# Kernel tuning notes

Measured on AMD Instinct MI355X. Metric: run time of the kernel, lower is better.

## Reference

```python
import jax, jax.numpy as jnp
import numpy as np

B, S, N, D, H, C, E, DG = 2, 512, 20000, 384, 3, 128, 320000, 128
NEG_SLOPE = 0.2  # PyG GATConv default


def setup_inputs() -> dict:
    key = jax.random.key(0)
    ks = jax.random.split(key, 10)
    p = lambda k, sh: jax.random.normal(k, sh, jnp.float32) * 0.02
    return dict(
        x_enc=jax.random.normal(ks[0], (B, S, D), jnp.float32),
        mask=jax.random.uniform(ks[1], (B, N), dtype=jnp.float32),
        edge_index=jax.random.randint(ks[2], (2, E), 0, N),
        Wq=p(ks[3], (N, S)), bq=jnp.zeros((N,), jnp.float32),
        Wm=p(ks[4], (D, 1)), bm=jnp.zeros((D,), jnp.float32),
        Wlin=p(ks[5], (H * C, D)),
        att_src=p(ks[6], (H, C)), att_dst=p(ks[7], (H, C)),
        bias_gat=jnp.zeros((H * C,), jnp.float32),
        Wproj=p(ks[8], (S, N)), bproj=jnp.zeros((S,), jnp.float32),
        Wtemp=p(ks[9], (DG, H * C)), btemp=jnp.zeros((DG,), jnp.float32),
    )


def reference(x_enc, mask, edge_index, Wq, bq, Wm, bm, Wlin, att_src, att_dst,
              bias_gat, Wproj, bproj, Wtemp, btemp):
    # q = query_proj(x_enc.permute(0,2,1)).permute(0,2,1)  -> [B, N, D]
    q = jnp.einsum('bsd,ns->bnd', x_enc, Wq) + bq[None, :, None]
    # mask_proj: Linear(1, D) on mask[..., None]  -> [B, N, D]
    mask_embed = mask[..., None] * Wm[:, 0] + bm
    x = (q + mask_embed).reshape(B * N, D)

    # batch edge_index with per-graph node offsets, then add self-loops (PyG default)
    offs = (jnp.arange(B, dtype=edge_index.dtype) * N)[:, None]
    src = (edge_index[0][None, :] + offs).reshape(-1)
    dst = (edge_index[1][None, :] + offs).reshape(-1)
    loops = jnp.arange(B * N, dtype=edge_index.dtype)
    src = jnp.concatenate([src, loops])
    dst = jnp.concatenate([dst, loops])

    # GATConv: shared linear, per-head attention
    xp = (x @ Wlin.T).reshape(B * N, H, C)                  # [BN, H, C]
    a_src = jnp.einsum('nhc,hc->nh', xp, att_src)           # [BN, H]
    a_dst = jnp.einsum('nhc,hc->nh', xp, att_dst)
    e = jax.nn.leaky_relu(a_src[src] + a_dst[dst], NEG_SLOPE)  # [Etot, H]
    # segment-softmax over incoming edges of each destination node
    emax = jax.ops.segment_max(e, dst, num_segments=B * N)
    ee = jnp.exp(e - emax[dst])
    denom = jax.ops.segment_sum(ee, dst, num_segments=B * N)
    alpha = ee / denom[dst]                                  # [Etot, H]
    out = jax.ops.segment_sum(xp[src] * alpha[..., None], dst, num_segments=B * N)
    out = out.reshape(B, N, H * C) + bias_gat                # concat heads + bias

    # dropout is identity in eval
    # project: Linear(N, S) over node dim -> [B, S, H*C]
    out = jnp.einsum('bnf,sn->bsf', out, Wproj) + bproj[None, :, None]
    # temp_project: Linear(H*C, d_graph)
    out = out @ Wtemp.T + btemp
    return out
```

## Files before the change

### kernel.cpp

```cpp
#include <hip/hip_runtime.h>
#include <hip/hip_bf16.h>
#include <cstdint>

#define B_   2
#define S_   512
#define N_   20000
#define H_   3
#define C_   128
#define E_   320000
#define DG_  128
#define D_   384
#define BN_  (B_ * N_)
#define F_   (H_ * C_)
#define ECSR_ (E_ + N_)

#define MPADQ 20096
#define MPADL 40064

#define PNS2 32
#define PCH2 640

using short8  = __attribute__((ext_vector_type(8))) short;
using floatx4 = __attribute__((ext_vector_type(4))) float;

__device__ __forceinline__ float b2f(unsigned short u) {
  union { unsigned int i; float f; } x; x.i = ((unsigned int)u) << 16; return x.f;
}
__device__ __forceinline__ unsigned short f2b(float f) {
  __hip_bfloat16 b = __float2bfloat16(f);
  return *reinterpret_cast<unsigned short*>(&b);
}

struct bf4 { __hip_bfloat16 a, b, c, d; };

#define NWQ4 ((MPADQ * 512) / 4)
#define NXE4 ((B_ * S_ * D_) / 4)
#define NWL4 ((F_ * D_) / 4)
#define NWP4 ((S_ * N_) / 4)
#define NWT4 ((DG_ * F_) / 4)
#define NCV0 NWQ4
#define NCV1 (NCV0 + NXE4)
#define NCV2 (NCV1 + NWL4)
#define NCV3 (NCV2 + NWP4)
#define NCV4 (NCV3 + NWT4)
#define NCVTOT (NCV4 + (F_ + DG_) * 64)

__device__ __forceinline__ void cv4(const float* __restrict__ src,
                                    __hip_bfloat16* __restrict__ dst, int e) {
  float4 v = *(const float4*)(src + e);
  bf4 r{__float2bfloat16(v.x), __float2bfloat16(v.y),
        __float2bfloat16(v.z), __float2bfloat16(v.w)};
  *(bf4*)(dst + e) = r;
}

__global__ __launch_bounds__(256) void conv_all_kernel(
    const float* __restrict__ Wq,    __hip_bfloat16* __restrict__ WqB,
    const float* __restrict__ xe,    __hip_bfloat16* __restrict__ xeB,
    const float* __restrict__ Wlin,  __hip_bfloat16* __restrict__ WlinB,
    const float* __restrict__ Wproj, __hip_bfloat16* __restrict__ WprojB,
    const float* __restrict__ Wtemp, __hip_bfloat16* __restrict__ WtempB,
    const float* __restrict__ Wm,    const float* __restrict__ bm,
    float* __restrict__ epi,         float* __restrict__ swt) {
  int idx = blockIdx.x * 256 + threadIdx.x;
  if (idx < NCV0) {
    int e = idx * 4;
    int row = e >> 9;
    float4 v = make_float4(0.f, 0.f, 0.f, 0.f);
    if (row < N_) v = *(const float4*)(Wq + e);
    bf4 r{__float2bfloat16(v.x), __float2bfloat16(v.y),
          __float2bfloat16(v.z), __float2bfloat16(v.w)};
    *(bf4*)(WqB + e) = r;
  } else if (idx < NCV1) {
    cv4(xe, xeB, (idx - NCV0) * 4);
  } else if (idx < NCV2) {
    cv4(Wlin, WlinB, (idx - NCV1) * 4);
  } else if (idx < NCV3) {
    cv4(Wproj, WprojB, (idx - NCV2) * 4);
  } else if (idx < NCV4) {
    cv4(Wtemp, WtempB, (idx - NCV3) * 4);
  } else {
    int w = (idx - NCV4) >> 6;
    int lane = idx & 63;
    if (w < F_) {
      float s0 = 0.f, s1 = 0.f, s2 = 0.f;
      const float* row = Wlin + (size_t)w * D_;
      for (int d = lane; d < D_; d += 64) {
        float wv = row[d];
        s0 += wv; s1 += Wm[d] * wv; s2 += bm[d] * wv;
      }
#pragma unroll
      for (int o = 32; o > 0; o >>= 1) {
        s0 += __shfl_down(s0, o); s1 += __shfl_down(s1, o); s2 += __shfl_down(s2, o);
      }
      if (lane == 0) { epi[w] = s0; epi[F_ + w] = s1; epi[2 * F_ + w] = s2; }
    } else {
      int g = w - F_;
      float s = 0.f;
      const float* row = Wtemp + (size_t)g * F_;
      for (int f = lane; f < F_; f += 64) s += row[f];
#pragma unroll
      for (int o = 32; o > 0; o >>= 1) s += __shfl_down(s, o);
      if (lane == 0) swt[g] = s;
    }
  }
}

template <int EPI>
__global__ __launch_bounds__(256) void mfma_gemm_nt(
    const __hip_bfloat16* __restrict__ A, const __hip_bfloat16* __restrict__ Bt,
    __hip_bfloat16* __restrict__ Cout, int K, int Mvalid, int ldc,
    size_t bstrideB, size_t bstrideC,
    const float* __restrict__ bq, const float* __restrict__ mask,
    const float* __restrict__ epi) {
  const int tid = threadIdx.x;
  const int m0 = blockIdx.x * 128;
  const int n0 = blockIdx.y * 128;
  const int bz = blockIdx.z;

  const unsigned short* Ap = (const unsigned short*)A;
  const unsigned short* Bp = (const unsigned short*)(Bt + bstrideB * bz);

  __shared__ __align__(16) unsigned short As[128][40];
  __shared__ __align__(16) unsigned short Bs[128][40];

  const int wave = tid >> 6, lane = tid & 63;
  const int wm = (wave & 1) * 64, wn = (wave >> 1) * 64;
  const int lrow = lane & 15, lk = (lane >> 4) * 8;

  const int srow = tid >> 2;
  const int skoff = (tid & 3) * 8;

  floatx4 acc[4][4];
#pragma unroll
  for (int i = 0; i < 4; ++i)
#pragma unroll
    for (int j = 0; j < 4; ++j) acc[i][j] = floatx4{0.f, 0.f, 0.f, 0.f};

  for (int k0 = 0; k0 < K; k0 += 32) {
    int4 av0 = *(const int4*)(Ap + (size_t)(m0 + srow) * K + k0 + skoff);
    int4 av1 = *(const int4*)(Ap + (size_t)(m0 + 64 + srow) * K + k0 + skoff);
    int4 bv0 = *(const int4*)(Bp + (size_t)(n0 + srow) * K + k0 + skoff);
    int4 bv1 = *(const int4*)(Bp + (size_t)(n0 + 64 + srow) * K + k0 + skoff);
    __syncthreads();
    *(int4*)&As[srow][skoff] = av0;
    *(int4*)&As[64 + srow][skoff] = av1;
    *(int4*)&Bs[srow][skoff] = bv0;
    *(int4*)&Bs[64 + srow][skoff] = bv1;
    __syncthreads();
    short8 af[4], bf[4];
#pragma unroll
    for (int mt = 0; mt < 4; ++mt)
      af[mt] = *(const short8*)&As[wm + mt * 16 + lrow][lk];
#pragma unroll
    for (int nt = 0; nt < 4; ++nt)
      bf[nt] = *(const short8*)&Bs[wn + nt * 16 + lrow][lk];
#pragma unroll
    for (int mt = 0; mt < 4; ++mt)
#pragma unroll
      for (int nt = 0; nt < 4; ++nt)
        acc[mt][nt] = __builtin_amdgcn_mfma_f32_16x16x32_bf16(af[mt], bf[nt],
                                                              acc[mt][nt], 0, 0, 0);
  }

  __hip_bfloat16* Cb = Cout + bstrideC * bz;
#pragma unroll
  for (int mt = 0; mt < 4; ++mt) {
#pragma unroll
    for (int r = 0; r < 4; ++r) {
      int rg = m0 + wm + mt * 16 + (lane >> 4) * 4 + r;
      if (rg < Mvalid) {
        float bqv = 0.f, mkv = 0.f;
        if (EPI) {
          bqv = bq[rg];
          mkv = mask[bz * N_ + rg];
        }
#pragma unroll
        for (int nt = 0; nt < 4; ++nt) {
          int cg = n0 + wn + nt * 16 + lrow;
          float v = acc[mt][nt][r];
          if (EPI) v += bqv * epi[cg] + mkv * epi[F_ + cg] + epi[2 * F_ + cg];
          Cb[(size_t)rg * ldc + cg] = __float2bfloat16(v);
        }
      }
    }
  }
}

__global__ __launch_bounds__(256) void gemm_gn(
    const __hip_bfloat16* __restrict__ A, const __hip_bfloat16* __restrict__ Bt,
    __hip_bfloat16* __restrict__ gnT) {
  const int tid = threadIdx.x;
  const int m0 = blockIdx.x * 128;

  const unsigned short* Ap = (const unsigned short*)A;
  const unsigned short* Bp = (const unsigned short*)Bt;

  __shared__ __align__(16) unsigned short As[128][40];
  __shared__ __align__(16) unsigned short Bs[128][40];

  const int wave = tid >> 6, lane = tid & 63;
  const int wm = (wave & 1) * 64, wn = (wave >> 1) * 64;
  const int lrow = lane & 15, lk = (lane >> 4) * 8;
  const int srow = tid >> 2;
  const int skoff = (tid & 3) * 8;

  floatx4 acc[4][4];
#pragma unroll
  for (int i = 0; i < 4; ++i)
#pragma unroll
    for (int j = 0; j < 4; ++j) acc[i][j] = floatx4{0.f, 0.f, 0.f, 0.f};

  for (int k0 = 0; k0 < F_; k0 += 32) {
    int4 av0 = *(const int4*)(Ap + (size_t)(m0 + srow) * F_ + k0 + skoff);
    int4 av1 = *(const int4*)(Ap + (size_t)(m0 + 64 + srow) * F_ + k0 + skoff);
    int4 bv0 = *(const int4*)(Bp + (size_t)(srow) * F_ + k0 + skoff);
    int4 bv1 = *(const int4*)(Bp + (size_t)(64 + srow) * F_ + k0 + skoff);
    __syncthreads();
    *(int4*)&As[srow][skoff] = av0;
    *(int4*)&As[64 + srow][skoff] = av1;
    *(int4*)&Bs[srow][skoff] = bv0;
    *(int4*)&Bs[64 + srow][skoff] = bv1;
    __syncthreads();
    short8 af[4], bf[4];
#pragma unroll
    for (int mt = 0; mt < 4; ++mt)
      af[mt] = *(const short8*)&As[wm + mt * 16 + lrow][lk];
#pragma unroll
    for (int nt = 0; nt < 4; ++nt)
      bf[nt] = *(const short8*)&Bs[wn + nt * 16 + lrow][lk];
#pragma unroll
    for (int mt = 0; mt < 4; ++mt)
#pragma unroll
      for (int nt = 0; nt < 4; ++nt)
        acc[mt][nt] = __builtin_amdgcn_mfma_f32_16x16x32_bf16(af[mt], bf[nt],
                                                              acc[mt][nt], 0, 0, 0);
  }

#pragma unroll
  for (int mt = 0; mt < 4; ++mt) {
    int rg0 = m0 + wm + mt * 16 + (lane >> 4) * 4;
    if (rg0 < BN_) {
      int b = (rg0 >= N_) ? 1 : 0;
      int n = rg0 - b * N_;
#pragma unroll
      for (int nt = 0; nt < 4; ++nt) {
        int cg = wn + nt * 16 + lrow;
        ushort4 o;
        o.x = f2b(acc[mt][nt][0]); o.y = f2b(acc[mt][nt][1]);
        o.z = f2b(acc[mt][nt][2]); o.w = f2b(acc[mt][nt][3]);
        *(ushort4*)((unsigned short*)gnT + (size_t)b * DG_ * N_ + (size_t)cg * N_ + n) = o;
      }
    }
  }
}

__global__ __launch_bounds__(256) void gemm_proj2(
    const __hip_bfloat16* __restrict__ A, const __hip_bfloat16* __restrict__ Bt,
    float* __restrict__ Ppart) {
  const int tid = threadIdx.x;
  const int m0 = blockIdx.x * 128;
  const int bz = blockIdx.z;
  const int b = bz / PNS2, ks = bz - b * PNS2;
  const int kbeg = ks * PCH2;
  const int kend = (kbeg + PCH2 < N_) ? (kbeg + PCH2) : N_;

  const unsigned short* Ap = (const unsigned short*)A;
  const unsigned short* Bp = (const unsigned short*)(Bt + (size_t)b * DG_ * N_);

  __shared__ __align__(16) unsigned short As[128][40];
  __shared__ __align__(16) unsigned short Bs[128][40];

  const int wave = tid >> 6, lane = tid & 63;
  const int wm = (wave & 1) * 64, wn = (wave >> 1) * 64;
  const int lrow = lane & 15, lk = (lane >> 4) * 8;
  const int srow = tid >> 2;
  const int skoff = (tid & 3) * 8;

  floatx4 acc[4][4];
#pragma unroll
  for (int i = 0; i < 4; ++i)
#pragma unroll
    for (int j = 0; j < 4; ++j) acc[i][j] = floatx4{0.f, 0.f, 0.f, 0.f};

  for (int k0 = kbeg; k0 < kend; k0 += 32) {
    int4 av0 = *(const int4*)(Ap + (size_t)(m0 + srow) * N_ + k0 + skoff);
    int4 av1 = *(const int4*)(Ap + (size_t)(m0 + 64 + srow) * N_ + k0 + skoff);
    int4 bv0 = *(const int4*)(Bp + (size_t)(srow) * N_ + k0 + skoff);
    int4 bv1 = *(const int4*)(Bp + (size_t)(64 + srow) * N_ + k0 + skoff);
    __syncthreads();
    *(int4*)&As[srow][skoff] = av0;
    *(int4*)&As[64 + srow][skoff] = av1;
    *(int4*)&Bs[srow][skoff] = bv0;
    *(int4*)&Bs[64 + srow][skoff] = bv1;
    __syncthreads();
    short8 af[4], bf[4];
#pragma unroll
    for (int mt = 0; mt < 4; ++mt)
      af[mt] = *(const short8*)&As[wm + mt * 16 + lrow][lk];
#pragma unroll
    for (int nt = 0; nt < 4; ++nt)
      bf[nt] = *(const short8*)&Bs[wn + nt * 16 + lrow][lk];
#pragma unroll
    for (int mt = 0; mt < 4; ++mt)
#pragma unroll
      for (int nt = 0; nt < 4; ++nt)
        acc[mt][nt] = __builtin_amdgcn_mfma_f32_16x16x32_bf16(af[mt], bf[nt],
                                                              acc[mt][nt], 0, 0, 0);
  }

  float* Pp = Ppart + (size_t)bz * S_ * DG_;
#pragma unroll
  for (int mt = 0; mt < 4; ++mt) {
#pragma unroll
    for (int r = 0; r < 4; ++r) {
      int rg = m0 + wm + mt * 16 + (lane >> 4) * 4 + r;
#pragma unroll
      for (int nt = 0; nt < 4; ++nt) {
        int cg = wn + nt * 16 + lrow;
        Pp[(size_t)rg * DG_ + cg] = acc[mt][nt][r];
      }
    }
  }
}

__global__ __launch_bounds__(256) void att_kernel(
    const __hip_bfloat16* __restrict__ xp, const float* __restrict__ att_src,
    const float* __restrict__ att_dst, float* __restrict__ a_src,
    float* __restrict__ a_dst) {
  int gid = blockIdx.x * blockDim.x + threadIdx.x;
  int wid = gid >> 6;
  int lane = threadIdx.x & 63;
  if (wid >= BN_ * H_) return;
  int i = wid / H_, h = wid - i * H_;
  const __hip_bfloat16* row = xp + (size_t)i * F_ + h * C_;
  const float* as = att_src + h * C_;
  const float* ad = att_dst + h * C_;
  float v0 = __bfloat162float(row[lane]), v1 = __bfloat162float(row[lane + 64]);
  float s1 = v0 * as[lane] + v1 * as[lane + 64];
  float s2 = v0 * ad[lane] + v1 * ad[lane + 64];
#pragma unroll
  for (int off = 32; off > 0; off >>= 1) {
    s1 += __shfl_down(s1, off);
    s2 += __shfl_down(s2, off);
  }
  if (lane == 0) {
    a_src[i * H_ + h] = s1;
    a_dst[i * H_ + h] = s2;
  }
}

__global__ __launch_bounds__(256) void count_kernel(const int* __restrict__ ei,
                                                    int* __restrict__ counts,
                                                    int* __restrict__ rank) {
  int idx = blockIdx.x * blockDim.x + threadIdx.x;
  if (idx >= E_) return;
  int d = ei[E_ + idx];
  rank[idx] = atomicAdd(&counts[d], 1);
}

#define SCB 1024
#define NSCB ((N_ + SCB - 1) / SCB)
__global__ __launch_bounds__(1024) void scan1_kernel(const int* __restrict__ counts,
                                                     int* __restrict__ offs,
                                                     int* __restrict__ btot) {
  __shared__ int wsum[16];
  int t = threadIdx.x, wave = t >> 6, lane = t & 63;
  int i = blockIdx.x * SCB + t;
  int v = (i < N_) ? (counts[i] + 1) : 0;
  int x = v;
#pragma unroll
  for (int o = 1; o < 64; o <<= 1) {
    int y = __shfl_up(x, o);
    if (lane >= o) x += y;
  }
  if (lane == 63) wsum[wave] = x;
  __syncthreads();
  if (wave == 0) {
    int w = (lane < 16) ? wsum[lane] : 0;
#pragma unroll
    for (int o = 1; o < 16; o <<= 1) {
      int y = __shfl_up(w, o);
      if (lane >= o) w += y;
    }
    if (lane < 16) wsum[lane] = w;
  }
  __syncthreads();
  int woff = (wave == 0) ? 0 : wsum[wave - 1];
  if (i < N_) offs[i] = woff + x - v;
  if (t == 0) btot[blockIdx.x] = wsum[15];
}

__global__ __launch_bounds__(64) void scan2_kernel(int* __restrict__ btot) {
  int lane = threadIdx.x;
  int v = (lane < NSCB) ? btot[lane] : 0;
  int x = v;
#pragma unroll
  for (int o = 1; o < 64; o <<= 1) {
    int y = __shfl_up(x, o);
    if (lane >= o) x += y;
  }
  if (lane < NSCB) btot[lane] = x - v;
}

__global__ __launch_bounds__(256) void scan3_kernel(int* __restrict__ offs,
                                                    const int* __restrict__ btot) {
  int i = blockIdx.x * 256 + threadIdx.x;
  if (i < N_) offs[i] += btot[i >> 10];
}

__global__ __launch_bounds__(256) void fill_kernel(
    const int* __restrict__ ei, const int* __restrict__ rank,
    const int* __restrict__ offs, const int* __restrict__ counts,
    int* __restrict__ col) {
  int idx = blockIdx.x * blockDim.x + threadIdx.x;
  if (idx >= ECSR_) return;
  if (idx < E_) {
    int sg = ei[idx];
    int dg = ei[E_ + idx];
    col[offs[dg] + rank[idx]] = sg;
  } else {
    int n = idx - E_;
    col[offs[n] + counts[n]] = n;
  }
}

__global__ __launch_bounds__(128) void agg_kernel(
    const int* __restrict__ offs, const int* __restrict__ counts,
    const int* __restrict__ col, const float* __restrict__ a_src,
    const float* __restrict__ a_dst, const __hip_bfloat16* __restrict__ xp,
    const float* __restrict__ bias_gat, __hip_bfloat16* __restrict__ out) {
  int bi = blockIdx.x;
  int q = (bi >= N_) ? 1 : 0;
  int n = bi - q * N_;
  int qn = q * N_;
  int i = qn + n;
  int t = threadIdx.x;
  if (t >= 96) return;
  int beg = offs[n];
  int nE = counts[n] + 1;
  int h = t >> 5;

  const ushort4* xp4 = (const ushort4*)xp;
  float ad = a_dst[(size_t)i * 3 + h];
  float ax = 0.f, ay = 0.f, az = 0.f, aw = 0.f, sw = 0.f;

  int j = 0;
  for (; j + 4 <= nE; j += 4) {
    int s0 = col[beg + j + 0] + qn;
    int s1 = col[beg + j + 1] + qn;
    int s2 = col[beg + j + 2] + qn;
    int s3 = col[beg + j + 3] + qn;
    float e0 = a_src[(size_t)s0 * 3 + h] + ad;
    float e1 = a_src[(size_t)s1 * 3 + h] + ad;
    float e2 = a_src[(size_t)s2 * 3 + h] + ad;
    float e3 = a_src[(size_t)s3 * 3 + h] + ad;
    e0 = (e0 > 0.f) ? e0 : 0.2f * e0;
    e1 = (e1 > 0.f) ? e1 : 0.2f * e1;
    e2 = (e2 > 0.f) ? e2 : 0.2f * e2;
    e3 = (e3 > 0.f) ? e3 : 0.2f * e3;
    float w0 = __expf(e0), w1 = __expf(e1);
    float w2 = __expf(e2), w3 = __expf(e3);
    sw += (w0 + w1) + (w2 + w3);
    ushort4 v0 = xp4[(size_t)s0 * 96 + t];
    ushort4 v1 = xp4[(size_t)s1 * 96 + t];
    ushort4 v2 = xp4[(size_t)s2 * 96 + t];
    ushort4 v3 = xp4[(size_t)s3 * 96 + t];
    ax = fmaf(w0, b2f(v0.x), ax); ay = fmaf(w0, b2f(v0.y), ay);
    az = fmaf(w0, b2f(v0.z), az); aw = fmaf(w0, b2f(v0.w), aw);
    ax = fmaf(w1, b2f(v1.x), ax); ay = fmaf(w1, b2f(v1.y), ay);
    az = fmaf(w1, b2f(v1.z), az); aw = fmaf(w1, b2f(v1.w), aw);
    ax = fmaf(w2, b2f(v2.x), ax); ay = fmaf(w2, b2f(v2.y), ay);
    az = fmaf(w2, b2f(v2.z), az); aw = fmaf(w2, b2f(v2.w), aw);
    ax = fmaf(w3, b2f(v3.x), ax); ay = fmaf(w3, b2f(v3.y), ay);
    az = fmaf(w3, b2f(v3.z), az); aw = fmaf(w3, b2f(v3.w), aw);
  }
  for (; j < nE; ++j) {
    int s0 = col[beg + j] + qn;
    float e0 = a_src[(size_t)s0 * 3 + h] + ad;
    e0 = (e0 > 0.f) ? e0 : 0.2f * e0;
    float w0 = __expf(e0);
    sw += w0;
    ushort4 v0 = xp4[(size_t)s0 * 96 + t];
    ax = fmaf(w0, b2f(v0.x), ax); ay = fmaf(w0, b2f(v0.y), ay);
    az = fmaf(w0, b2f(v0.z), az); aw = fmaf(w0, b2f(v0.w), aw);
  }

  float r = 1.0f / sw;
  const float4 bg = *(const float4*)(bias_gat + t * 4);
  ushort4 o;
  o.x = f2b(ax * r + bg.x);
  o.y = f2b(ay * r + bg.y);
  o.z = f2b(az * r + bg.z);
  o.w = f2b(aw * r + bg.w);
  *(ushort4*)((unsigned short*)out + (size_t)i * F_ + t * 4) = o;
}

__global__ __launch_bounds__(128) void final_kernel(
    const float* __restrict__ Ppart, const float* __restrict__ bproj,
    const float* __restrict__ swt, const float* __restrict__ btemp,
    float* __restrict__ out) {
  int bs = blockIdx.x;
  int b = bs >> 9;
  int s = bs & (S_ - 1);
  int g = threadIdx.x;
  float acc = btemp[g] + bproj[s] * swt[g];
  const float* pp = Ppart + ((size_t)b * PNS2 * S_ + s) * DG_ + g;
  for (int ns = 0; ns < PNS2; ++ns) acc += pp[(size_t)ns * S_ * DG_];
  out[(size_t)bs * DG_ + g] = acc;
}

extern "C" void kernel_launch(void* const* d_in, const int* in_sizes, int n_in,
                              void* d_out, int out_size, void* d_ws, size_t ws_size,
                              hipStream_t stream) {
  const float* x_enc   = (const float*)d_in[0];
  const float* mask    = (const float*)d_in[1];
  const int*   ei      = (const int*)d_in[2];
  const float* Wq      = (const float*)d_in[3];
  const float* bq      = (const float*)d_in[4];
  const float* Wm      = (const float*)d_in[5];
  const float* bm      = (const float*)d_in[6];
  const float* Wlin    = (const float*)d_in[7];
  const float* att_src = (const float*)d_in[8];
  const float* att_dst = (const float*)d_in[9];
  const float* bias_gat= (const float*)d_in[10];
  const float* Wproj   = (const float*)d_in[11];
  const float* bproj   = (const float*)d_in[12];
  const float* Wtemp   = (const float*)d_in[13];
  const float* btemp   = (const float*)d_in[14];
  float* outp = (float*)d_out;

  char* ws = (char*)d_ws;
  size_t off = 0;
  auto alloc = [&](size_t bytes) {
    char* p = ws + off;
    off = (off + bytes + 255) & ~(size_t)255;
    return p;
  };

  const size_t GNT_OFF = (size_t)B_ * PNS2 * S_ * DG_ * 4;
  char* regionA = alloc(GNT_OFF + (size_t)B_ * DG_ * N_ * 2);
  __hip_bfloat16* Wq_b = (__hip_bfloat16*)regionA;
  float* Ppart = (float*)regionA;
  __hip_bfloat16* gnT  = (__hip_bfloat16*)(regionA + GNT_OFF);

  __hip_bfloat16* xeB    = (__hip_bfloat16*)alloc((size_t)B_ * S_ * D_ * 2);
  __hip_bfloat16* yT     = (__hip_bfloat16*)alloc((size_t)B_ * F_ * S_ * 2);
  __hip_bfloat16* xp     = (__hip_bfloat16*)alloc((size_t)BN_ * F_ * 2);
  __hip_bfloat16* gat    = (__hip_bfloat16*)alloc((size_t)MPADL * F_ * 2);
  __hip_bfloat16* WlinB  = (__hip_bfloat16*)alloc((size_t)F_ * D_ * 2);
  __hip_bfloat16* WprojB = (__hip_bfloat16*)alloc((size_t)S_ * N_ * 2);
  __hip_bfloat16* WtempB = (__hip_bfloat16*)alloc((size_t)DG_ * F_ * 2);
  float* epi   = (float*)alloc((size_t)3 * F_ * 4);
  float* swt   = (float*)alloc((size_t)DG_ * 4);
  float* a_src = (float*)alloc((size_t)BN_ * H_ * 4);
  float* a_dst = (float*)alloc((size_t)BN_ * H_ * 4);
  int* counts  = (int*)alloc((size_t)N_ * 4);
  int* offsb   = (int*)alloc((size_t)N_ * 4);
  int* rank    = (int*)alloc((size_t)E_ * 4);
  int* col     = (int*)alloc((size_t)ECSR_ * 4);
  int* btot    = (int*)alloc((size_t)NSCB * 4);
  if (off > ws_size) return;

  hipMemsetAsync(counts, 0, (size_t)N_ * 4, stream);
  hipMemsetAsync(gat + (size_t)BN_ * F_, 0, (size_t)(MPADL - BN_) * F_ * 2, stream);

  count_kernel<<<(E_ + 255) / 256, 256, 0, stream>>>(ei, counts, rank);
  scan1_kernel<<<NSCB, SCB, 0, stream>>>(counts, offsb, btot);
  scan2_kernel<<<1, 64, 0, stream>>>(btot);
  scan3_kernel<<<(N_ + 255) / 256, 256, 0, stream>>>(offsb, btot);
  fill_kernel<<<(ECSR_ + 255) / 256, 256, 0, stream>>>(ei, rank, offsb, counts, col);

  conv_all_kernel<<<NCVTOT / 256, 256, 0, stream>>>(
      Wq, Wq_b, x_enc, xeB, Wlin, WlinB, Wproj, WprojB, Wtemp, WtempB,
      Wm, bm, epi, swt);

  mfma_gemm_nt<0><<<dim3(F_ / 128, S_ / 128, B_), 256, 0, stream>>>(
      WlinB, xeB, yT, D_, F_, S_, (size_t)S_ * D_, (size_t)F_ * S_,
      nullptr, nullptr, nullptr);
  mfma_gemm_nt<1><<<dim3(MPADQ / 128, F_ / 128, B_), 256, 0, stream>>>(
      Wq_b, yT, xp, S_, N_, F_, (size_t)F_ * S_, (size_t)N_ * F_,
      bq, mask, epi);

  att_kernel<<<(BN_ * H_ + 3) / 4, 256, 0, stream>>>(xp, att_src, att_dst, a_src, a_dst);
  agg_kernel<<<BN_, 128, 0, stream>>>(offsb, counts, col, a_src, a_dst,
                                      xp, bias_gat, gat);

  gemm_gn<<<dim3(MPADL / 128, 1, 1), 256, 0, stream>>>(gat, WtempB, gnT);
  gemm_proj2<<<dim3(S_ / 128, 1, B_ * PNS2), 256, 0, stream>>>(WprojB, gnT, Ppart);
  final_kernel<<<B_ * S_, 128, 0, stream>>>(Ppart, bproj, swt, btemp, outp);
}
```

Measured before the change: 354.8 us.

## Fuse Wq conversion and attention logits into the Q GEMM; pack agg blocks

The Q-projection GEMM now reads fp32 Wq directly and converts it to bf16 in registers, so the separate padded Wq conversion pass and its workspace round trip go away. The same kernel's epilogue computes the per-head a_src and a_dst dot products with shuffle reductions and atomics into zeroed buffers, which removes the separate att_kernel and its re-read of xp. The aggregation kernel now handles two nodes per 192-thread block instead of leaving 32 of 128 threads idle. In exchange the GEMM reloads fp32 Wq (twice the bytes of bf16) and adds atomics, and atomic accumulation makes the logits depend on summation order.

```diff
diff --git a/kernel.cpp b/kernel.cpp
--- a/kernel.cpp
+++ b/kernel.cpp
@@ -33,17 +33,15 @@
 
 struct bf4 { __hip_bfloat16 a, b, c, d; };
 
-#define NWQ4 ((MPADQ * 512) / 4)
 #define NXE4 ((B_ * S_ * D_) / 4)
 #define NWL4 ((F_ * D_) / 4)
 #define NWP4 ((S_ * N_) / 4)
 #define NWT4 ((DG_ * F_) / 4)
-#define NCV0 NWQ4
-#define NCV1 (NCV0 + NXE4)
-#define NCV2 (NCV1 + NWL4)
-#define NCV3 (NCV2 + NWP4)
-#define NCV4 (NCV3 + NWT4)
-#define NCVTOT (NCV4 + (F_ + DG_) * 64)
+#define NCV0 NXE4
+#define NCV1 (NCV0 + NWL4)
+#define NCV2 (NCV1 + NWP4)
+#define NCV3 (NCV2 + NWT4)
+#define NCVTOT (NCV3 + (F_ + DG_) * 64)
 
 __device__ __forceinline__ void cv4(const float* __restrict__ src,
                                     __hip_bfloat16* __restrict__ dst, int e) {
@@ -54,7 +52,6 @@
 }
 
 __global__ __launch_bounds__(256) void conv_all_kernel(
-    const float* __restrict__ Wq,    __hip_bfloat16* __restrict__ WqB,
     const float* __restrict__ xe,    __hip_bfloat16* __restrict__ xeB,
     const float* __restrict__ Wlin,  __hip_bfloat16* __restrict__ WlinB,
     const float* __restrict__ Wproj, __hip_bfloat16* __restrict__ WprojB,
@@ -63,23 +60,15 @@
     float* __restrict__ epi,         float* __restrict__ swt) {
   int idx = blockIdx.x * 256 + threadIdx.x;
   if (idx < NCV0) {
-    int e = idx * 4;
-    int row = e >> 9;
-    float4 v = make_float4(0.f, 0.f, 0.f, 0.f);
-    if (row < N_) v = *(const float4*)(Wq + e);
-    bf4 r{__float2bfloat16(v.x), __float2bfloat16(v.y),
-          __float2bfloat16(v.z), __float2bfloat16(v.w)};
-    *(bf4*)(WqB + e) = r;
+    cv4(xe, xeB, idx * 4);
   } else if (idx < NCV1) {
-    cv4(xe, xeB, (idx - NCV0) * 4);
+    cv4(Wlin, WlinB, (idx - NCV0) * 4);
   } else if (idx < NCV2) {
-    cv4(Wlin, WlinB, (idx - NCV1) * 4);
+    cv4(Wproj, WprojB, (idx - NCV1) * 4);
   } else if (idx < NCV3) {
-    cv4(Wproj, WprojB, (idx - NCV2) * 4);
-  } else if (idx < NCV4) {
-    cv4(Wtemp, WtempB, (idx - NCV3) * 4);
+    cv4(Wtemp, WtempB, (idx - NCV2) * 4);
   } else {
-    int w = (idx - NCV4) >> 6;
+    int w = (idx - NCV3) >> 6;
     int lane = idx & 63;
     if (w < F_) {
       float s0 = 0.f, s1 = 0.f, s2 = 0.f;
@@ -105,13 +94,10 @@
   }
 }
 
-template <int EPI>
 __global__ __launch_bounds__(256) void mfma_gemm_nt(
     const __hip_bfloat16* __restrict__ A, const __hip_bfloat16* __restrict__ Bt,
     __hip_bfloat16* __restrict__ Cout, int K, int Mvalid, int ldc,
-    size_t bstrideB, size_t bstrideC,
-    const float* __restrict__ bq, const float* __restrict__ mask,
-    const float* __restrict__ epi) {
+    size_t bstrideB, size_t bstrideC) {
   const int tid = threadIdx.x;
   const int m0 = blockIdx.x * 128;
   const int n0 = blockIdx.y * 128;
@@ -126,7 +112,6 @@
   const int wave = tid >> 6, lane = tid & 63;
   const int wm = (wave & 1) * 64, wn = (wave >> 1) * 64;
   const int lrow = lane & 15, lk = (lane >> 4) * 8;
-
   const int srow = tid >> 2;
   const int skoff = (tid & 3) * 8;
 
@@ -169,18 +154,127 @@
     for (int r = 0; r < 4; ++r) {
       int rg = m0 + wm + mt * 16 + (lane >> 4) * 4 + r;
       if (rg < Mvalid) {
-        float bqv = 0.f, mkv = 0.f;
-        if (EPI) {
-          bqv = bq[rg];
-          mkv = mask[bz * N_ + rg];
-        }
 #pragma unroll
         for (int nt = 0; nt < 4; ++nt) {
           int cg = n0 + wn + nt * 16 + lrow;
-          float v = acc[mt][nt][r];
-          if (EPI) v += bqv * epi[cg] + mkv * epi[F_ + cg] + epi[2 * F_ + cg];
-          Cb[(size_t)rg * ldc + cg] = __float2bfloat16(v);
+          Cb[(size_t)rg * ldc + cg] = __float2bfloat16(acc[mt][nt][r]);
         }
+      }
+    }
+  }
+}
+
+__global__ __launch_bounds__(256) void gemm_q_att(
+    const float* __restrict__ Wq, const __hip_bfloat16* __restrict__ yT,
+    __hip_bfloat16* __restrict__ xp,
+    const float* __restrict__ bq, const float* __restrict__ mask,
+    const float* __restrict__ epi,
+    const float* __restrict__ att_src, const float* __restrict__ att_dst,
+    float* __restrict__ a_src, float* __restrict__ a_dst) {
+  const int tid = threadIdx.x;
+  const int m0 = blockIdx.x * 128;
+  const int n0 = blockIdx.y * 128;
+  const int bz = blockIdx.z;
+  const int hh = n0 >> 7;
+
+  const unsigned short* Bp = (const unsigned short*)(yT + (size_t)bz * F_ * S_);
+
+  __shared__ __align__(16) unsigned short As[128][40];
+  __shared__ __align__(16) unsigned short Bs[128][40];
+
+  const int wave = tid >> 6, lane = tid & 63;
+  const int wm = (wave & 1) * 64, wn = (wave >> 1) * 64;
+  const int lrow = lane & 15, lk = (lane >> 4) * 8;
+  const int srow = tid >> 2;
+  const int skoff = (tid & 3) * 8;
+
+  const int rowA0 = m0 + srow, rowA1 = m0 + 64 + srow;
+  const bool vA0 = rowA0 < N_, vA1 = rowA1 < N_;
+
+  floatx4 acc[4][4];
+#pragma unroll
+  for (int i = 0; i < 4; ++i)
+#pragma unroll
+    for (int j = 0; j < 4; ++j) acc[i][j] = floatx4{0.f, 0.f, 0.f, 0.f};
+
+  for (int k0 = 0; k0 < S_; k0 += 32) {
+    float4 z = make_float4(0.f, 0.f, 0.f, 0.f);
+    float4 a0l = z, a0h = z, a1l = z, a1h = z;
+    if (vA0) {
+      const float* p = Wq + (size_t)rowA0 * S_ + k0 + skoff;
+      a0l = *(const float4*)p; a0h = *(const float4*)(p + 4);
+    }
+    if (vA1) {
+      const float* p = Wq + (size_t)rowA1 * S_ + k0 + skoff;
+      a1l = *(const float4*)p; a1h = *(const float4*)(p + 4);
+    }
+    int4 bv0 = *(const int4*)(Bp + (size_t)(n0 + srow) * S_ + k0 + skoff);
+    int4 bv1 = *(const int4*)(Bp + (size_t)(n0 + 64 + srow) * S_ + k0 + skoff);
+    short8 a0v, a1v;
+    a0v[0] = (short)f2b(a0l.x); a0v[1] = (short)f2b(a0l.y);
+    a0v[2] = (short)f2b(a0l.z); a0v[3] = (short)f2b(a0l.w);
+    a0v[4] = (short)f2b(a0h.x); a0v[5] = (short)f2b(a0h.y);
+    a0v[6] = (short)f2b(a0h.z); a0v[7] = (short)f2b(a0h.w);
+    a1v[0] = (short)f2b(a1l.x); a1v[1] = (short)f2b(a1l.y);
+    a1v[2] = (short)f2b(a1l.z); a1v[3] = (short)f2b(a1l.w);
+    a1v[4] = (short)f2b(a1h.x); a1v[5] = (short)f2b(a1h.y);
+    a1v[6] = (short)f2b(a1h.z); a1v[7] = (short)f2b(a1h.w);
+    __syncthreads();
+    *(short8*)&As[srow][skoff] = a0v;
+    *(short8*)&As[64 + srow][skoff] = a1v;
+    *(int4*)&Bs[srow][skoff] = bv0;
+    *(int4*)&Bs[64 + srow][skoff] = bv1;
+    __syncthreads();
+    short8 af[4], bf[4];
+#pragma unroll
+    for (int mt = 0; mt < 4; ++mt)
+      af[mt] = *(const short8*)&As[wm + mt * 16 + lrow][lk];
+#pragma unroll
+    for (int nt = 0; nt < 4; ++nt)
+      bf[nt] = *(const short8*)&Bs[wn + nt * 16 + lrow][lk];
+#pragma unroll
+    for (int mt = 0; mt < 4; ++mt)
+#pragma unroll
+      for (int nt = 0; nt < 4; ++nt)
+        acc[mt][nt] = __builtin_amdgcn_mfma_f32_16x16x32_bf16(af[mt], bf[nt],
+                                                              acc[mt][nt], 0, 0, 0);
+  }
+
+  __hip_bfloat16* Cb = xp + (size_t)bz * N_ * F_;
+  const float* asp = att_src + hh * C_;
+  const float* adp = att_dst + hh * C_;
+  float asv[4], adv[4], e0v[4], e1v[4], e2v[4];
+#pragma unroll
+  for (int nt = 0; nt < 4; ++nt) {
+    int cc = wn + nt * 16 + lrow;
+    int cg = n0 + cc;
+    asv[nt] = asp[cc]; adv[nt] = adp[cc];
+    e0v[nt] = epi[cg]; e1v[nt] = epi[F_ + cg]; e2v[nt] = epi[2 * F_ + cg];
+  }
+#pragma unroll
+  for (int mt = 0; mt < 4; ++mt) {
+#pragma unroll
+    for (int r = 0; r < 4; ++r) {
+      int rg = m0 + wm + mt * 16 + (lane >> 4) * 4 + r;
+      bool valid = rg < N_;
+      float bqv = 0.f, mkv = 0.f;
+      if (valid) { bqv = bq[rg]; mkv = mask[bz * N_ + rg]; }
+      float s1 = 0.f, s2 = 0.f;
+#pragma unroll
+      for (int nt = 0; nt < 4; ++nt) {
+        float v = acc[mt][nt][r] + bqv * e0v[nt] + mkv * e1v[nt] + e2v[nt];
+        if (valid) Cb[(size_t)rg * F_ + n0 + wn + nt * 16 + lrow] = __float2bfloat16(v);
+        s1 = fmaf(v, asv[nt], s1);
+        s2 = fmaf(v, adv[nt], s2);
+      }
+#pragma unroll
+      for (int o = 8; o > 0; o >>= 1) {
+        s1 += __shfl_down(s1, o, 16);
+        s2 += __shfl_down(s2, o, 16);
+      }
+      if (valid && lrow == 0) {
+        atomicAdd(&a_src[(size_t)(bz * N_ + rg) * 3 + hh], s1);
+        atomicAdd(&a_dst[(size_t)(bz * N_ + rg) * 3 + hh], s2);
       }
     }
   }
@@ -320,32 +414,6 @@
         Pp[(size_t)rg * DG_ + cg] = acc[mt][nt][r];
       }
     }
-  }
-}
-
-__global__ __launch_bounds__(256) void att_kernel(
-    const __hip_bfloat16* __restrict__ xp, const float* __restrict__ att_src,
-    const float* __restrict__ att_dst, float* __restrict__ a_src,
-    float* __restrict__ a_dst) {
-  int gid = blockIdx.x * blockDim.x + threadIdx.x;
-  int wid = gid >> 6;
-  int lane = threadIdx.x & 63;
-  if (wid >= BN_ * H_) return;
-  int i = wid / H_, h = wid - i * H_;
-  const __hip_bfloat16* row = xp + (size_t)i * F_ + h * C_;
-  const float* as = att_src + h * C_;
-  const float* ad = att_dst + h * C_;
-  float v0 = __bfloat162float(row[lane]), v1 = __bfloat162float(row[lane + 64]);
-  float s1 = v0 * as[lane] + v1 * as[lane + 64];
-  float s2 = v0 * ad[lane] + v1 * ad[lane + 64];
-#pragma unroll
-  for (int off = 32; off > 0; off >>= 1) {
-    s1 += __shfl_down(s1, off);
-    s2 += __shfl_down(s2, off);
-  }
-  if (lane == 0) {
-    a_src[i * H_ + h] = s1;
-    a_dst[i * H_ + h] = s2;
   }
 }
 
@@ -424,21 +492,23 @@
   }
 }
 
-__global__ __launch_bounds__(128) void agg_kernel(
+__global__ __launch_bounds__(192) void agg_kernel(
     const int* __restrict__ offs, const int* __restrict__ counts,
     const int* __restrict__ col, const float* __restrict__ a_src,
     const float* __restrict__ a_dst, const __hip_bfloat16* __restrict__ xp,
     const float* __restrict__ bias_gat, __hip_bfloat16* __restrict__ out) {
   int bi = blockIdx.x;
-  int q = (bi >= N_) ? 1 : 0;
-  int n = bi - q * N_;
+  int q = (bi >= N_ / 2) ? 1 : 0;
+  int pb = bi - q * (N_ / 2);
+  int t = threadIdx.x;
+  int half = (t >= 96) ? 1 : 0;
+  int tt = t - half * 96;
+  int n = pb * 2 + half;
   int qn = q * N_;
   int i = qn + n;
-  int t = threadIdx.x;
-  if (t >= 96) return;
   int beg = offs[n];
   int nE = counts[n] + 1;
-  int h = t >> 5;
+  int h = tt >> 5;
 
   const ushort4* xp4 = (const ushort4*)xp;
   float ad = a_dst[(size_t)i * 3 + h];
@@ -461,10 +531,10 @@
     float w0 = __expf(e0), w1 = __expf(e1);
     float w2 = __expf(e2), w3 = __expf(e3);
     sw += (w0 + w1) + (w2 + w3);
-    ushort4 v0 = xp4[(size_t)s0 * 96 + t];
-    ushort4 v1 = xp4[(size_t)s1 * 96 + t];
-    ushort4 v2 = xp4[(size_t)s2 * 96 + t];
-    ushort4 v3 = xp4[(size_t)s3 * 96 + t];
+    ushort4 v0 = xp4[(size_t)s0 * 96 + tt];
+    ushort4 v1 = xp4[(size_t)s1 * 96 + tt];
+    ushort4 v2 = xp4[(size_t)s2 * 96 + tt];
+    ushort4 v3 = xp4[(size_t)s3 * 96 + tt];
     ax = fmaf(w0, b2f(v0.x), ax); ay = fmaf(w0, b2f(v0.y), ay);
     az = fmaf(w0, b2f(v0.z), az); aw = fmaf(w0, b2f(v0.w), aw);
     ax = fmaf(w1, b2f(v1.x), ax); ay = fmaf(w1, b2f(v1.y), ay);
@@ -480,19 +550,19 @@
     e0 = (e0 > 0.f) ? e0 : 0.2f * e0;
     float w0 = __expf(e0);
     sw += w0;
-    ushort4 v0 = xp4[(size_t)s0 * 96 + t];
+    ushort4 v0 = xp4[(size_t)s0 * 96 + tt];
     ax = fmaf(w0, b2f(v0.x), ax); ay = fmaf(w0, b2f(v0.y), ay);
     az = fmaf(w0, b2f(v0.z), az); aw = fmaf(w0, b2f(v0.w), aw);
   }
 
   float r = 1.0f / sw;
-  const float4 bg = *(const float4*)(bias_gat + t * 4);
+  const float4 bg = *(const float4*)(bias_gat + tt * 4);
   ushort4 o;
   o.x = f2b(ax * r + bg.x);
   o.y = f2b(ay * r + bg.y);
   o.z = f2b(az * r + bg.z);
   o.w = f2b(aw * r + bg.w);
-  *(ushort4*)((unsigned short*)out + (size_t)i * F_ + t * 4) = o;
+  *(ushort4*)((unsigned short*)out + (size_t)i * F_ + tt * 4) = o;
 }
 
 __global__ __launch_bounds__(128) void final_kernel(
@@ -539,7 +609,6 @@
 
   const size_t GNT_OFF = (size_t)B_ * PNS2 * S_ * DG_ * 4;
   char* regionA = alloc(GNT_OFF + (size_t)B_ * DG_ * N_ * 2);
-  __hip_bfloat16* Wq_b = (__hip_bfloat16*)regionA;
   float* Ppart = (float*)regionA;
   __hip_bfloat16* gnT  = (__hip_bfloat16*)(regionA + GNT_OFF);
 
@@ -562,6 +631,7 @@
   if (off > ws_size) return;
 
   hipMemsetAsync(counts, 0, (size_t)N_ * 4, stream);
+  hipMemsetAsync(a_src, 0, (size_t)2 * BN_ * H_ * 4, stream);
   hipMemsetAsync(gat + (size_t)BN_ * F_, 0, (size_t)(MPADL - BN_) * F_ * 2, stream);
 
   count_kernel<<<(E_ + 255) / 256, 256, 0, stream>>>(ei, counts, rank);
@@ -571,19 +641,16 @@
   fill_kernel<<<(ECSR_ + 255) / 256, 256, 0, stream>>>(ei, rank, offsb, counts, col);
 
   conv_all_kernel<<<NCVTOT / 256, 256, 0, stream>>>(
-      Wq, Wq_b, x_enc, xeB, Wlin, WlinB, Wproj, WprojB, Wtemp, WtempB,
+      x_enc, xeB, Wlin, WlinB, Wproj, WprojB, Wtemp, WtempB,
       Wm, bm, epi, swt);
 
-  mfma_gemm_nt<0><<<dim3(F_ / 128, S_ / 128, B_), 256, 0, stream>>>(
-      WlinB, xeB, yT, D_, F_, S_, (size_t)S_ * D_, (size_t)F_ * S_,
-      nullptr, nullptr, nullptr);
-  mfma_gemm_nt<1><<<dim3(MPADQ / 128, F_ / 128, B_), 256, 0, stream>>>(
-      Wq_b, yT, xp, S_, N_, F_, (size_t)F_ * S_, (size_t)N_ * F_,
-      bq, mask, epi);
-
-  att_kernel<<<(BN_ * H_ + 3) / 4, 256, 0, stream>>>(xp, att_src, att_dst, a_src, a_dst);
-  agg_kernel<<<BN_, 128, 0, stream>>>(offsb, counts, col, a_src, a_dst,
-                                      xp, bias_gat, gat);
+  mfma_gemm_nt<<<dim3(F_ / 128, S_ / 128, B_), 256, 0, stream>>>(
+      WlinB, xeB, yT, D_, F_, S_, (size_t)S_ * D_, (size_t)F_ * S_);
+  gemm_q_att<<<dim3(MPADQ / 128, F_ / 128, B_), 256, 0, stream>>>(
+      Wq, yT, xp, bq, mask, epi, att_src, att_dst, a_src, a_dst);
+
+  agg_kernel<<<BN_ / 2, 192, 0, stream>>>(offsb, counts, col, a_src, a_dst,
+                                          xp, bias_gat, gat);
 
   gemm_gn<<<dim3(MPADL / 128, 1, 1), 256, 0, stream>>>(gat, WtempB, gnT);
   gemm_proj2<<<dim3(S_ / 128, 1, B_ * PNS2), 256, 0, stream>>>(WprojB, gnT, Ppart);
```

Measured after the change: 378.7 us. 1.07x slower.

## Reduce split-K projection with atomics and unroll aggregation loop by eight

Applied to the files above, without the earlier changes.

The split-K projection GEMM now atomically adds its partial tiles straight into the output. A small init kernel first seeds the output with the bias terms, and the Ppart buffer and final reduction kernel are removed, saving the partial-sum write and read-back traffic. The GAT aggregation kernel gains an 8-way unrolled edge loop that batches index, attention and feature loads so more memory requests are in flight. The trade-off is atomic contention, since 32 K-splits hit each output element, plus nondeterministic summation order.

```diff
diff --git a/kernel.cpp b/kernel.cpp
--- a/kernel.cpp
+++ b/kernel.cpp
@@ -256,7 +256,7 @@
 
 __global__ __launch_bounds__(256) void gemm_proj2(
     const __hip_bfloat16* __restrict__ A, const __hip_bfloat16* __restrict__ Bt,
-    float* __restrict__ Ppart) {
+    float* __restrict__ out) {
   const int tid = threadIdx.x;
   const int m0 = blockIdx.x * 128;
   const int bz = blockIdx.z;
@@ -308,7 +308,7 @@
                                                               acc[mt][nt], 0, 0, 0);
   }
 
-  float* Pp = Ppart + (size_t)bz * S_ * DG_;
+  float* op = out + (size_t)b * S_ * DG_;
 #pragma unroll
   for (int mt = 0; mt < 4; ++mt) {
 #pragma unroll
@@ -317,10 +317,19 @@
 #pragma unroll
       for (int nt = 0; nt < 4; ++nt) {
         int cg = wn + nt * 16 + lrow;
-        Pp[(size_t)rg * DG_ + cg] = acc[mt][nt][r];
+        atomicAdd(&op[(size_t)rg * DG_ + cg], acc[mt][nt][r]);
       }
     }
   }
+}
+
+__global__ __launch_bounds__(128) void init_out_kernel(
+    const float* __restrict__ bproj, const float* __restrict__ swt,
+    const float* __restrict__ btemp, float* __restrict__ out) {
+  int bs = blockIdx.x;
+  int s = bs & (S_ - 1);
+  int g = threadIdx.x;
+  out[(size_t)bs * DG_ + g] = btemp[g] + bproj[s] * swt[g];
 }
 
 __global__ __launch_bounds__(256) void att_kernel(
@@ -445,6 +454,27 @@
   float ax = 0.f, ay = 0.f, az = 0.f, aw = 0.f, sw = 0.f;
 
   int j = 0;
+  for (; j + 8 <= nE; j += 8) {
+    int s[8];
+    float w[8];
+    ushort4 v[8];
+#pragma unroll
+    for (int u = 0; u < 8; ++u) s[u] = col[beg + j + u] + qn;
+#pragma unroll
+    for (int u = 0; u < 8; ++u) {
+      float e = a_src[(size_t)s[u] * 3 + h] + ad;
+      e = (e > 0.f) ? e : 0.2f * e;
+      w[u] = __expf(e);
+    }
+#pragma unroll
+    for (int u = 0; u < 8; ++u) v[u] = xp4[(size_t)s[u] * 96 + t];
+#pragma unroll
+    for (int u = 0; u < 8; ++u) {
+      sw += w[u];
+      ax = fmaf(w[u], b2f(v[u].x), ax); ay = fmaf(w[u], b2f(v[u].y), ay);
+      az = fmaf(w[u], b2f(v[u].z), az); aw = fmaf(w[u], b2f(v[u].w), aw);
+    }
+  }
   for (; j + 4 <= nE; j += 4) {
     int s0 = col[beg + j + 0] + qn;
     int s1 = col[beg + j + 1] + qn;
@@ -495,20 +525,6 @@
   *(ushort4*)((unsigned short*)out + (size_t)i * F_ + t * 4) = o;
 }
 
-__global__ __launch_bounds__(128) void final_kernel(
-    const float* __restrict__ Ppart, const float* __restrict__ bproj,
-    const float* __restrict__ swt, const float* __restrict__ btemp,
-    float* __restrict__ out) {
-  int bs = blockIdx.x;
-  int b = bs >> 9;
-  int s = bs & (S_ - 1);
-  int g = threadIdx.x;
-  float acc = btemp[g] + bproj[s] * swt[g];
-  const float* pp = Ppart + ((size_t)b * PNS2 * S_ + s) * DG_ + g;
-  for (int ns = 0; ns < PNS2; ++ns) acc += pp[(size_t)ns * S_ * DG_];
-  out[(size_t)bs * DG_ + g] = acc;
-}
-
 extern "C" void kernel_launch(void* const* d_in, const int* in_sizes, int n_in,
                               void* d_out, int out_size, void* d_ws, size_t ws_size,
                               hipStream_t stream) {
@@ -537,11 +553,9 @@
     return p;
   };
 
-  const size_t GNT_OFF = (size_t)B_ * PNS2 * S_ * DG_ * 4;
-  char* regionA = alloc(GNT_OFF + (size_t)B_ * DG_ * N_ * 2);
+  char* regionA = alloc((size_t)MPADQ * S_ * 2);
   __hip_bfloat16* Wq_b = (__hip_bfloat16*)regionA;
-  float* Ppart = (float*)regionA;
-  __hip_bfloat16* gnT  = (__hip_bfloat16*)(regionA + GNT_OFF);
+  __hip_bfloat16* gnT  = (__hip_bfloat16*)regionA;
 
   __hip_bfloat16* xeB    = (__hip_bfloat16*)alloc((size_t)B_ * S_ * D_ * 2);
   __hip_bfloat16* yT     = (__hip_bfloat16*)alloc((size_t)B_ * F_ * S_ * 2);
@@ -586,6 +600,6 @@
                                       xp, bias_gat, gat);
 
   gemm_gn<<<dim3(MPADL / 128, 1, 1), 256, 0, stream>>>(gat, WtempB, gnT);
-  gemm_proj2<<<dim3(S_ / 128, 1, B_ * PNS2), 256, 0, stream>>>(WprojB, gnT, Ppart);
-  final_kernel<<<B_ * S_, 128, 0, stream>>>(Ppart, bproj, swt, btemp, outp);
-}
+  init_out_kernel<<<B_ * S_, 128, 0, stream>>>(bproj, swt, btemp, outp);
+  gemm_proj2<<<dim3(S_ / 128, 1, B_ * PNS2), 256, 0, stream>>>(WprojB, gnT, outp);
+}
```

Result: slower. 369.1 us (+4.0%).
